# Optimization experiments

Measured on AMD Instinct MI355X. Metric: run time of the kernel, lower is better.

The kernel has to match this reference:

```python
import jax, jax.numpy as jnp
import numpy as np

B, T, C = 2, 2048, 1024
NH = 16
DFF = 4096
EPS = 1e-5


def setup_inputs() -> dict:
    key = jax.random.key(0)
    ks = jax.random.split(key, 12)
    s = 0.02
    return {
        "x": jax.random.normal(ks[0], (B, T, C), dtype=jnp.float32),
        "Wq": jax.random.normal(ks[1], (C, C), dtype=jnp.float32) * s,
        "bq": jax.random.normal(ks[2], (C,), dtype=jnp.float32) * s,
        "Wk": jax.random.normal(ks[3], (C, C), dtype=jnp.float32) * s,
        "bk": jax.random.normal(ks[4], (C,), dtype=jnp.float32) * s,
        "Wv": jax.random.normal(ks[5], (C, C), dtype=jnp.float32) * s,
        "bv": jax.random.normal(ks[6], (C,), dtype=jnp.float32) * s,
        "W1": jax.random.normal(ks[7], (C, DFF), dtype=jnp.float32) * s,
        "b1": jax.random.normal(ks[8], (DFF,), dtype=jnp.float32) * s,
        "W2": jax.random.normal(ks[9], (DFF, C), dtype=jnp.float32) * s,
        "b2": jax.random.normal(ks[10], (C,), dtype=jnp.float32) * s,
        "ln_w": jnp.ones((C,), dtype=jnp.float32),
    }


def _layernorm(x, w):
    # LayerNorm over last dim, weight only (bias=False), eps=1e-5
    mu = jnp.mean(x, axis=-1, keepdims=True)
    var = jnp.mean(jnp.square(x - mu), axis=-1, keepdims=True)
    return (x - mu) / jnp.sqrt(var + EPS) * w


def reference(x, Wq, bq, Wk, bk, Wv, bv, W1, b1, W2, b2, ln_w):
    Bx, Tx, Cx = x.shape
    hd = Cx // NH
    q = (x @ Wq + bq).reshape(Bx, Tx, NH, hd).transpose(0, 2, 1, 3)  # [B,H,T,hd]
    k = (x @ Wk + bk).reshape(Bx, Tx, NH, hd).transpose(0, 2, 1, 3)
    v = (x @ Wv + bv).reshape(Bx, Tx, NH, hd).transpose(0, 2, 1, 3)
    # NOTE: original scales by sqrt(d_k) = sqrt(FULL model dim C), not head dim
    scores = jnp.einsum("bhqd,bhkd->bhqk", q, k) / jnp.sqrt(jnp.float32(Cx))
    causal = jnp.tril(jnp.ones((Tx, Tx), dtype=bool))
    scores = jnp.where(causal[None, None, :, :], scores, -jnp.inf)
    attn = jax.nn.softmax(scores, axis=-1)
    head_out = jnp.einsum("bhqk,bhkd->bhqd", attn, v)
    a = head_out.transpose(0, 2, 1, 3).reshape(Bx, Tx, Cx)
    # residuals: out = x + ln(x) with SHARED ln weight
    h = a + _layernorm(a, ln_w)
    f = jax.nn.relu(h @ W1 + b1) @ W2 + b2
    out = f + _layernorm(f, ln_w)
    return out
```

## Files before the change

kernel.cpp:

```cpp
#include <hip/hip_runtime.h>
#include <math.h>


typedef __attribute__((ext_vector_type(8))) short short8;
typedef __attribute__((ext_vector_type(4))) float f32x4;

__device__ __forceinline__ unsigned short f2bf(float f) {
    unsigned u = __builtin_bit_cast(unsigned, f);
    unsigned r = u + 0x7fffu + ((u >> 16) & 1u);
    return (unsigned short)(r >> 16);
}

__global__ __launch_bounds__(256) void prep_kernel(
    const float* __restrict__ x,  const float* __restrict__ Wq,
    const float* __restrict__ Wk, const float* __restrict__ Wv,
    const float* __restrict__ W1, const float* __restrict__ W2,
    const float* __restrict__ bq, const float* __restrict__ bk,
    unsigned short* __restrict__ x_bf,  unsigned short* __restrict__ Wqk_t,
    unsigned short* __restrict__ Wvt,   unsigned short* __restrict__ W1t,
    unsigned short* __restrict__ W2t,   float* __restrict__ bqk)
{
    const int bid = blockIdx.x;
    const int tid = threadIdx.x;

    if (bid < 4096) {
        const int i = (bid * 256 + tid) * 4;
        float4 v = *(const float4*)(x + i);
        ushort4 o;
        o.x = f2bf(v.x); o.y = f2bf(v.y); o.z = f2bf(v.z); o.w = f2bf(v.w);
        *(ushort4*)(x_bf + i) = o;
        return;
    }
    if (bid >= 15360) {
        const int i = (bid - 15360) * 256 + tid;
        bqk[i] = i < 1024 ? bq[i] : bk[i - 1024];
        return;
    }

    __shared__ float tile[32][33];
    const float* src; unsigned short* dst; int K, N, t;
    if (bid < 5120)       { t = bid - 4096;  src = Wq; dst = Wqk_t;            K = 1024; N = 1024; }
    else if (bid < 6144)  { t = bid - 5120;  src = Wk; dst = Wqk_t + 1048576;  K = 1024; N = 1024; }
    else if (bid < 7168)  { t = bid - 6144;  src = Wv; dst = Wvt;              K = 1024; N = 1024; }
    else if (bid < 11264) { t = bid - 7168;  src = W1; dst = W1t;              K = 1024; N = 4096; }
    else                  { t = bid - 11264; src = W2; dst = W2t;              K = 4096; N = 1024; }

    const int ncols = N >> 5;
    const int n0 = (t % ncols) * 32;
    const int k0 = (t / ncols) * 32;
    const int tx = tid & 31;
    const int ty = tid >> 5;
#pragma unroll
    for (int i = 0; i < 4; ++i)
        tile[ty + i * 8][tx] = src[(size_t)(k0 + ty + i * 8) * N + n0 + tx];
    __syncthreads();
#pragma unroll
    for (int i = 0; i < 4; ++i)
        dst[(size_t)(n0 + ty + i * 8) * K + k0 + tx] = f2bf(tile[tx][ty + i * 8]);
}

template <int TM, int TN, int NP>
__device__ __forceinline__ void gemm_body(
    unsigned short* AsB, unsigned short* BsB,
    const unsigned short* __restrict__ A, const unsigned short* __restrict__ Bt,
    const float* __restrict__ bias, float* __restrict__ Cf,
    unsigned short* __restrict__ Cb, int M, int N, int K, int mode,
    int bx, int by)
{
    constexpr int NI   = TM / 32;
    constexpr int NJ   = TN / 32;
    constexpr int NCA  = TM / 16;
    constexpr int NCB  = TN / 16;
    constexpr int MAXA = (NCA + 3) / 4;
    constexpr int MAXB = (NCB + 3) / 4;

    const int tid  = threadIdx.x;
    const int lane = tid & 63;
    const int w    = tid >> 6;
    const int wm   = (w & 1) * (TM / 2);
    const int wn   = (w >> 1) * (TN / 2);
    const int fm   = lane & 15;
    const int quad = lane >> 4;

    const int row0 = by * TM;
    const int col0 = bx * TN;

    const int srow = lane >> 2;
    const int scol = (lane & 3) * 8;

    const unsigned short* aptr[MAXA];
    int aoff[MAXA];
#pragma unroll
    for (int i = 0; i < MAXA; ++i) {
        const int c = w + i * 4;
        if (c < NCA) {
            aptr[i] = A + (size_t)(row0 + c * 16 + srow) * K + scol;
            aoff[i] = c * 16 * 32;
        }
    }
    const unsigned short* bptr[MAXB];
    int boff[MAXB];
#pragma unroll
    for (int i = 0; i < MAXB; ++i) {
        const int c = w + i * 4;
        if (c < NCB) {
            bptr[i] = Bt + (size_t)(col0 + c * 16 + srow) * K + scol;
            boff[i] = c * 16 * 32;
        }
    }

    f32x4 acc[NI][NJ] = {};

    for (int k0 = 0; k0 < K; k0 += NP * 32) {
        __syncthreads();
#pragma unroll
        for (int p = 0; p < NP; ++p) {
#pragma unroll
            for (int i = 0; i < MAXA; ++i)
                if (w + i * 4 < NCA)
                    __builtin_amdgcn_global_load_lds(
                        (const __attribute__((address_space(1))) void*)(aptr[i] + k0 + p * 32),
                        (__attribute__((address_space(3))) void*)&AsB[p * TM * 32 + aoff[i]], 16, 0, 0);
#pragma unroll
            for (int i = 0; i < MAXB; ++i)
                if (w + i * 4 < NCB)
                    __builtin_amdgcn_global_load_lds(
                        (const __attribute__((address_space(1))) void*)(bptr[i] + k0 + p * 32),
                        (__attribute__((address_space(3))) void*)&BsB[p * TN * 32 + boff[i]], 16, 0, 0);
        }
        __syncthreads();

#pragma unroll
        for (int p = 0; p < NP; ++p) {
            short8 af[NI], bf[NJ];
#pragma unroll
            for (int i = 0; i < NI; ++i)
                af[i] = *(const short8*)&AsB[p * TM * 32 + (wm + i * 16 + fm) * 32 + quad * 8];
#pragma unroll
            for (int j = 0; j < NJ; ++j)
                bf[j] = *(const short8*)&BsB[p * TN * 32 + (wn + j * 16 + fm) * 32 + quad * 8];
#pragma unroll
            for (int i = 0; i < NI; ++i)
#pragma unroll
                for (int j = 0; j < NJ; ++j)
                    acc[i][j] = __builtin_amdgcn_mfma_f32_16x16x32_bf16(
                        af[i], bf[j], acc[i][j], 0, 0, 0);
        }
    }

#pragma unroll
    for (int j = 0; j < NJ; ++j) {
        const int col = col0 + wn + j * 16 + fm;
        const float bcol = (mode == 3) ? 0.f : bias[col];
#pragma unroll
        for (int i = 0; i < NI; ++i) {
            const int rbase = row0 + wm + i * 16 + quad * 4;
#pragma unroll
            for (int r = 0; r < 4; ++r) {
                const int row = rbase + r;
                float val = acc[i][j][r] + ((mode == 3) ? bias[row] : bcol);
                if (mode == 1) val = fmaxf(val, 0.f);
                if (mode == 0) Cf[(size_t)row * N + col] = val;
                else           Cb[(size_t)row * N + col] = f2bf(val);
            }
        }
    }
}

template <int TM, int TN, int NP>
__global__ __launch_bounds__(256) void gemm_bf16_mfma(
    const unsigned short* __restrict__ A, const unsigned short* __restrict__ Bt,
    const float* __restrict__ bias, float* __restrict__ Cf,
    unsigned short* __restrict__ Cb, int M, int N, int K, int mode)
{
    __shared__ unsigned short As[NP * TM * 32];
    __shared__ unsigned short Bs[NP * TN * 32];
    gemm_body<TM, TN, NP>(As, Bs, A, Bt, bias, Cf, Cb, M, N, K, mode,
                          blockIdx.x, blockIdx.y);
}

template <int TM, int TN, int NP>
__global__ __launch_bounds__(256) void gemm_xcd(
    const unsigned short* __restrict__ A, const unsigned short* __restrict__ Bt,
    const float* __restrict__ bias, float* __restrict__ Cf,
    unsigned short* __restrict__ Cb, int M, int N, int K, int mode,
    int nx, int rows_per_xcd)
{
    __shared__ unsigned short As[NP * TM * 32];
    __shared__ unsigned short Bs[NP * TN * 32];
    const int xcd = blockIdx.x & 7;
    const int idx = blockIdx.x >> 3;
    const int bx  = idx % nx;
    const int by  = xcd * rows_per_xcd + idx / nx;
    gemm_body<TM, TN, NP>(As, Bs, A, Bt, bias, Cf, Cb, M, N, K, mode, bx, by);
}

template <int TM, int TN, int NP>
__global__ __launch_bounds__(256) void gemm_dual(
    const unsigned short* __restrict__ A0, const unsigned short* __restrict__ B0,
    const float* __restrict__ bias0, unsigned short* __restrict__ C0,
    int M0, int N0, int K0, int mode0, int nb0, int nx0,
    const unsigned short* __restrict__ A1, const unsigned short* __restrict__ B1,
    const float* __restrict__ bias1, unsigned short* __restrict__ C1,
    int M1, int N1, int K1, int mode1, int nx1)
{
    __shared__ unsigned short As[NP * TM * 32];
    __shared__ unsigned short Bs[NP * TN * 32];
    const int bid = blockIdx.x;
    if (bid < nb0) {
        gemm_body<TM, TN, NP>(As, Bs, A0, B0, bias0, nullptr, C0,
                              M0, N0, K0, mode0, bid % nx0, bid / nx0);
    } else {
        const int t = bid - nb0;
        gemm_body<TM, TN, NP>(As, Bs, A1, B1, bias1, nullptr, C1,
                              M1, N1, K1, mode1, t % nx1, t / nx1);
    }
}

__global__ __launch_bounds__(256) void fattn_mfma(
    const unsigned short* __restrict__ qk,
    const unsigned short* __restrict__ vt,
    float* __restrict__ a)
{
    const int T = 2048, LDQK = 2048, LDVT = 4096, OUTC = 1024;
    const float cs = 0.04508422f;

    __shared__ unsigned short Qs[2][64][32];
    __shared__ unsigned short Ks[2][64][32];
    __shared__ unsigned short Vs[2][64][32];
    __shared__ unsigned short Ps[4][16][72];

    const int tid  = threadIdx.x;
    const int lane = tid & 63;
    const int w    = tid >> 6;
    const int fm   = lane & 15;
    const int quad = lane >> 4;
    const int srow = lane >> 2;
    const int scol = (lane & 3) * 8;

    const int n  = blockIdx.x;
    const int lo = n & 255, hi = n >> 8;
    const int h  = ((lo >> 5) & 7) | ((hi & 1) << 3);
    const int b  = hi >> 1;
    const int qv = lo & 31;
    const int u  = ((qv & 1) << 4) | ((qv & 2) << 2) | (qv & 4) |
                   ((qv & 8) >> 2) | ((qv & 16) >> 4);
    const int qb = (hi & 1) ? (31 - u) : u;
    const int q0 = qb * 64;

    const size_t rowbase = (size_t)b * T;

#pragma unroll
    for (int i = 0; i < 2; ++i) {
        const int c  = w * 2 + i;
        const int kh = c & 1, rg = c >> 1;
        const unsigned short* src = qk + (rowbase + q0 + rg * 16 + srow) * LDQK
                                       + h * 64 + kh * 32 + scol;
        __builtin_amdgcn_global_load_lds(
            (const __attribute__((address_space(1))) void*)src,
            (__attribute__((address_space(3))) void*)&Qs[kh][rg * 16][0], 16, 0, 0);
    }
    __syncthreads();
    short8 qf0 = *(const short8*)&Qs[0][w * 16 + fm][quad * 8];
    short8 qf1 = *(const short8*)&Qs[1][w * 16 + fm][quad * 8];

    short8 ones;
#pragma unroll
    for (int i = 0; i < 8; ++i) ones[i] = (short)0x3F80;

    f32x4 o[4] = {};
    f32x4 lacc = {};

    const int qglob = q0 + w * 16 + fm;

    for (int jt = 0; jt <= qb; ++jt) {
        const int j0 = jt * 64;
        __syncthreads();
#pragma unroll
        for (int i = 0; i < 2; ++i) {
            const int c  = w * 2 + i;
            const int kh = c & 1, rg = c >> 1;
            const unsigned short* ksrc = qk + (rowbase + j0 + rg * 16 + srow) * LDQK
                                            + 1024 + h * 64 + kh * 32 + scol;
            __builtin_amdgcn_global_load_lds(
                (const __attribute__((address_space(1))) void*)ksrc,
                (__attribute__((address_space(3))) void*)&Ks[kh][rg * 16][0], 16, 0, 0);
            const unsigned short* vsrc = vt + (size_t)(h * 64 + rg * 16 + srow) * LDVT
                                            + rowbase + j0 + kh * 32 + scol;
            __builtin_amdgcn_global_load_lds(
                (const __attribute__((address_space(1))) void*)vsrc,
                (__attribute__((address_space(3))) void*)&Vs[kh][rg * 16][0], 16, 0, 0);
        }
        __syncthreads();

        f32x4 s[4];
#pragma unroll
        for (int j = 0; j < 4; ++j) {
            short8 k0 = *(const short8*)&Ks[0][j * 16 + fm][quad * 8];
            short8 k1 = *(const short8*)&Ks[1][j * 16 + fm][quad * 8];
            f32x4 acc = {};
            acc = __builtin_amdgcn_mfma_f32_16x16x32_bf16(k0, qf0, acc, 0, 0, 0);
            acc = __builtin_amdgcn_mfma_f32_16x16x32_bf16(k1, qf1, acc, 0, 0, 0);
            s[j] = acc;
        }

        if (jt == qb) {
#pragma unroll
            for (int j = 0; j < 4; ++j) {
                const int kbase = j0 + j * 16 + quad * 4;
#pragma unroll
                for (int r = 0; r < 4; ++r) {
                    const float e = exp2f(s[j][r] * cs);
                    s[j][r] = (kbase + r > qglob) ? 0.f : e;
                }
            }
        } else {
#pragma unroll
            for (int j = 0; j < 4; ++j)
#pragma unroll
                for (int r = 0; r < 4; ++r)
                    s[j][r] = exp2f(s[j][r] * cs);
        }

#pragma unroll
        for (int j = 0; j < 4; ++j) {
            const unsigned d0 = (unsigned)f2bf(s[j][0]) | ((unsigned)f2bf(s[j][1]) << 16);
            const unsigned d1 = (unsigned)f2bf(s[j][2]) | ((unsigned)f2bf(s[j][3]) << 16);
            *(uint2*)&Ps[w][fm][j * 16 + quad * 4] = make_uint2(d0, d1);
        }
        short8 pf0 = *(const short8*)&Ps[w][fm][quad * 8];
        short8 pf1 = *(const short8*)&Ps[w][fm][32 + quad * 8];

#pragma unroll
        for (int jd = 0; jd < 4; ++jd) {
            short8 v0 = *(const short8*)&Vs[0][jd * 16 + fm][quad * 8];
            short8 v1 = *(const short8*)&Vs[1][jd * 16 + fm][quad * 8];
            o[jd] = __builtin_amdgcn_mfma_f32_16x16x32_bf16(pf0, v0, o[jd], 0, 0, 0);
            o[jd] = __builtin_amdgcn_mfma_f32_16x16x32_bf16(pf1, v1, o[jd], 0, 0, 0);
        }
        lacc = __builtin_amdgcn_mfma_f32_16x16x32_bf16(pf0, ones, lacc, 0, 0, 0);
        lacc = __builtin_amdgcn_mfma_f32_16x16x32_bf16(pf1, ones, lacc, 0, 0, 0);
    }

    const size_t orow = rowbase + q0 + w * 16 + quad * 4;
#pragma unroll
    for (int r = 0; r < 4; ++r) {
        const float inv = 1.0f / lacc[r];
#pragma unroll
        for (int jd = 0; jd < 4; ++jd)
            a[(orow + r) * OUTC + h * 64 + jd * 16 + fm] = o[jd][r] * inv;
    }
}

__global__ __launch_bounds__(256) void add_ln_kernel(
    const float* __restrict__ in, const float* __restrict__ w,
    float* __restrict__ outf, unsigned short* __restrict__ outb, int bf16_out)
{
    const int C = 1024;
    const int row = blockIdx.x;
    const int tid = threadIdx.x;

    __shared__ float red[256];

    const float* x = in + (size_t)row * C;
    float4 xv = *(const float4*)(x + tid * 4);

    red[tid] = xv.x + xv.y + xv.z + xv.w;
    __syncthreads();
    for (int off = 128; off > 0; off >>= 1) {
        if (tid < off) red[tid] += red[tid + off];
        __syncthreads();
    }
    const float mu = red[0] * (1.0f / 1024.0f);
    __syncthreads();

    float dx = xv.x - mu, dy = xv.y - mu, dz = xv.z - mu, dw = xv.w - mu;
    red[tid] = dx * dx + dy * dy + dz * dz + dw * dw;
    __syncthreads();
    for (int off = 128; off > 0; off >>= 1) {
        if (tid < off) red[tid] += red[tid + off];
        __syncthreads();
    }
    const float rstd = rsqrtf(red[0] * (1.0f / 1024.0f) + 1e-5f);

    float4 wv = *(const float4*)(w + tid * 4);
    float ox = xv.x + dx * rstd * wv.x;
    float oy = xv.y + dy * rstd * wv.y;
    float oz = xv.z + dz * rstd * wv.z;
    float ow = xv.w + dw * rstd * wv.w;
    if (bf16_out) {
        ushort4 o4;
        o4.x = f2bf(ox); o4.y = f2bf(oy); o4.z = f2bf(oz); o4.w = f2bf(ow);
        *(ushort4*)(outb + (size_t)row * C + tid * 4) = o4;
    } else {
        *(float4*)(outf + (size_t)row * C + tid * 4) = make_float4(ox, oy, oz, ow);
    }
}

extern "C" void kernel_launch(void* const* d_in, const int* in_sizes, int n_in,
                              void* d_out, int out_size, void* d_ws, size_t ws_size,
                              hipStream_t stream)
{
    const float* x    = (const float*)d_in[0];
    const float* Wq   = (const float*)d_in[1];
    const float* bq   = (const float*)d_in[2];
    const float* Wk   = (const float*)d_in[3];
    const float* bk   = (const float*)d_in[4];
    const float* Wv   = (const float*)d_in[5];
    const float* bv   = (const float*)d_in[6];
    const float* W1   = (const float*)d_in[7];
    const float* b1   = (const float*)d_in[8];
    const float* W2   = (const float*)d_in[9];
    const float* b2   = (const float*)d_in[10];
    const float* ln_w = (const float*)d_in[11];
    float* out = (float*)d_out;
    char* ws = (char*)d_ws;

    const int B = 2, T = 2048, C = 1024, DFF = 4096;
    const int M = B * T;
    const size_t MB = 1048576;

    unsigned short* qk_bf = (unsigned short*)(ws);
    unsigned short* vt_bf = (unsigned short*)(ws + 16 * MB);
    float*          a     = (float*)(ws + 24 * MB);
    unsigned short* x_bf  = (unsigned short*)(ws + 40 * MB);
    unsigned short* Wqk_t = (unsigned short*)(ws + 48 * MB);
    unsigned short* Wvt   = (unsigned short*)(ws + 52 * MB);
    unsigned short* W1t   = (unsigned short*)(ws + 54 * MB);
    unsigned short* W2t   = (unsigned short*)(ws + 62 * MB);
    float*          bqk   = (float*)(ws + 70 * MB);
    unsigned short* u_bf  = (unsigned short*)(ws + 71 * MB);
    unsigned short* h_bf  = x_bf;
    float*          f     = (float*)(ws);

    dim3 blk(256);

    prep_kernel<<<dim3(15368), blk, 0, stream>>>(
        x, Wq, Wk, Wv, W1, W2, bq, bk,
        x_bf, Wqk_t, Wvt, W1t, W2t, bqk);

    gemm_dual<64, 64, 2><<<dim3(3072), blk, 0, stream>>>(
        x_bf, Wqk_t, bqk, qk_bf, M, 2 * C, C, 2, 2048, 32,
        Wvt, x_bf, bv, vt_bf, C, M, C, 3, 64);

    fattn_mfma<<<dim3(1024), blk, 0, stream>>>(qk_bf, vt_bf, a);

    add_ln_kernel<<<dim3(M), blk, 0, stream>>>(a, ln_w, nullptr, h_bf, 1);

    gemm_bf16_mfma<64, 128, 2><<<dim3(DFF / 128, M / 64), blk, 0, stream>>>(
        h_bf, W1t, b1, nullptr, u_bf, M, DFF, C, 1);

    gemm_xcd<128, 64, 4><<<dim3(512), blk, 0, stream>>>(
        u_bf, W2t, b2, f, nullptr, M, C, DFF, 0, 16, 4);

    add_ln_kernel<<<dim3(M), blk, 0, stream>>>(f, ln_w, out, nullptr, 0);
}
```

Before: 332.4 us.

## Enlarge GEMM tiles, add XCD-aware 2D tiling and split-K for FFN down projection

All GEMMs move to 128x128 tiles. The up projection gets an XCD-aware rectangular block mapping so each chiplet reuses a compact region of A and B. The down projection is split into two K halves that write separate fp32 buffers, and the final LayerNorm sums those halves before normalizing. The goal is more MFMA work per LDS load and better L2 locality, at the cost of fewer blocks per GEMM and an extra fp32 partial buffer to read and write.

```diff
diff --git a/kernel.cpp b/kernel.cpp
--- a/kernel.cpp
+++ b/kernel.cpp
@@ -65,7 +65,7 @@
     const unsigned short* __restrict__ A, const unsigned short* __restrict__ Bt,
     const float* __restrict__ bias, float* __restrict__ Cf,
     unsigned short* __restrict__ Cb, int M, int N, int K, int mode,
-    int bx, int by)
+    int bx, int by, int kbeg, int kend)
 {
     constexpr int NI   = TM / 32;
     constexpr int NJ   = TN / 32;
@@ -111,7 +111,7 @@
 
     f32x4 acc[NI][NJ] = {};
 
-    for (int k0 = 0; k0 < K; k0 += NP * 32) {
+    for (int k0 = kbeg; k0 < kend; k0 += NP * 32) {
         __syncthreads();
 #pragma unroll
         for (int p = 0; p < NP; ++p) {
@@ -151,7 +151,7 @@
 #pragma unroll
     for (int j = 0; j < NJ; ++j) {
         const int col = col0 + wn + j * 16 + fm;
-        const float bcol = (mode == 3) ? 0.f : bias[col];
+        const float bcol = (mode == 3 || mode == 4) ? 0.f : bias[col];
 #pragma unroll
         for (int i = 0; i < NI; ++i) {
             const int rbase = row0 + wm + i * 16 + quad * 4;
@@ -160,39 +160,50 @@
                 const int row = rbase + r;
                 float val = acc[i][j][r] + ((mode == 3) ? bias[row] : bcol);
                 if (mode == 1) val = fmaxf(val, 0.f);
-                if (mode == 0) Cf[(size_t)row * N + col] = val;
-                else           Cb[(size_t)row * N + col] = f2bf(val);
+                if (mode == 0 || mode == 4) Cf[(size_t)row * N + col] = val;
+                else                        Cb[(size_t)row * N + col] = f2bf(val);
             }
         }
     }
 }
 
 template <int TM, int TN, int NP>
-__global__ __launch_bounds__(256) void gemm_bf16_mfma(
-    const unsigned short* __restrict__ A, const unsigned short* __restrict__ Bt,
-    const float* __restrict__ bias, float* __restrict__ Cf,
-    unsigned short* __restrict__ Cb, int M, int N, int K, int mode)
-{
-    __shared__ unsigned short As[NP * TM * 32];
-    __shared__ unsigned short Bs[NP * TN * 32];
-    gemm_body<TM, TN, NP>(As, Bs, A, Bt, bias, Cf, Cb, M, N, K, mode,
-                          blockIdx.x, blockIdx.y);
-}
-
-template <int TM, int TN, int NP>
-__global__ __launch_bounds__(256) void gemm_xcd(
+__global__ __launch_bounds__(256) void gemm_xcd2(
     const unsigned short* __restrict__ A, const unsigned short* __restrict__ Bt,
     const float* __restrict__ bias, float* __restrict__ Cf,
     unsigned short* __restrict__ Cb, int M, int N, int K, int mode,
-    int nx, int rows_per_xcd)
+    int rw, int rh, int nrx)
 {
     __shared__ unsigned short As[NP * TM * 32];
     __shared__ unsigned short Bs[NP * TN * 32];
     const int xcd = blockIdx.x & 7;
     const int idx = blockIdx.x >> 3;
-    const int bx  = idx % nx;
-    const int by  = xcd * rows_per_xcd + idx / nx;
-    gemm_body<TM, TN, NP>(As, Bs, A, Bt, bias, Cf, Cb, M, N, K, mode, bx, by);
+    const int rx  = xcd % nrx;
+    const int ry  = xcd / nrx;
+    const int bx  = rx * rw + idx % rw;
+    const int by  = ry * rh + idx / rw;
+    gemm_body<TM, TN, NP>(As, Bs, A, Bt, bias, Cf, Cb, M, N, K, mode,
+                          bx, by, 0, K);
+}
+
+template <int TM, int TN, int NP>
+__global__ __launch_bounds__(256) void gemm_splitk(
+    const unsigned short* __restrict__ A, const unsigned short* __restrict__ Bt,
+    const float* __restrict__ bias, float* __restrict__ C0,
+    float* __restrict__ C1, int M, int N, int K,
+    int nxh, int rows_per_xcd_h, int nbh)
+{
+    __shared__ unsigned short As[NP * TM * 32];
+    __shared__ unsigned short Bs[NP * TN * 32];
+    const int half = blockIdx.x >= nbh;
+    const int r    = blockIdx.x - (half ? nbh : 0);
+    const int xcd  = blockIdx.x & 7;
+    const int idx  = r >> 3;
+    const int bx   = idx % nxh;
+    const int by   = xcd * rows_per_xcd_h + idx / nxh;
+    const int kb   = half ? (K >> 1) : 0;
+    gemm_body<TM, TN, NP>(As, Bs, A, Bt, bias, half ? C1 : C0, nullptr,
+                          M, N, K, half ? 4 : 0, bx, by, kb, kb + (K >> 1));
 }
 
 template <int TM, int TN, int NP>
@@ -209,11 +220,11 @@
     const int bid = blockIdx.x;
     if (bid < nb0) {
         gemm_body<TM, TN, NP>(As, Bs, A0, B0, bias0, nullptr, C0,
-                              M0, N0, K0, mode0, bid % nx0, bid / nx0);
+                              M0, N0, K0, mode0, bid % nx0, bid / nx0, 0, K0);
     } else {
         const int t = bid - nb0;
         gemm_body<TM, TN, NP>(As, Bs, A1, B1, bias1, nullptr, C1,
-                              M1, N1, K1, mode1, t % nx1, t / nx1);
+                              M1, N1, K1, mode1, t % nx1, t / nx1, 0, K1);
     }
 }
 
@@ -353,7 +364,8 @@
 }
 
 __global__ __launch_bounds__(256) void add_ln_kernel(
-    const float* __restrict__ in, const float* __restrict__ w,
+    const float* __restrict__ in, const float* __restrict__ in2,
+    const float* __restrict__ w,
     float* __restrict__ outf, unsigned short* __restrict__ outb, int bf16_out)
 {
     const int C = 1024;
@@ -364,6 +376,10 @@
 
     const float* x = in + (size_t)row * C;
     float4 xv = *(const float4*)(x + tid * 4);
+    if (in2) {
+        float4 yv = *(const float4*)(in2 + (size_t)row * C + tid * 4);
+        xv.x += yv.x; xv.y += yv.y; xv.z += yv.z; xv.w += yv.w;
+    }
 
     red[tid] = xv.x + xv.y + xv.z + xv.w;
     __syncthreads();
@@ -432,6 +448,7 @@
     unsigned short* u_bf  = (unsigned short*)(ws + 71 * MB);
     unsigned short* h_bf  = x_bf;
     float*          f     = (float*)(ws);
+    float*          f2    = a;
 
     dim3 blk(256);
 
@@ -439,19 +456,19 @@
         x, Wq, Wk, Wv, W1, W2, bq, bk,
         x_bf, Wqk_t, Wvt, W1t, W2t, bqk);
 
-    gemm_dual<64, 64, 2><<<dim3(3072), blk, 0, stream>>>(
-        x_bf, Wqk_t, bqk, qk_bf, M, 2 * C, C, 2, 2048, 32,
-        Wvt, x_bf, bv, vt_bf, C, M, C, 3, 64);
+    gemm_dual<128, 128, 2><<<dim3(768), blk, 0, stream>>>(
+        x_bf, Wqk_t, bqk, qk_bf, M, 2 * C, C, 2, 512, 16,
+        Wvt, x_bf, bv, vt_bf, C, M, C, 3, 32);
 
     fattn_mfma<<<dim3(1024), blk, 0, stream>>>(qk_bf, vt_bf, a);
 
-    add_ln_kernel<<<dim3(M), blk, 0, stream>>>(a, ln_w, nullptr, h_bf, 1);
-
-    gemm_bf16_mfma<64, 128, 2><<<dim3(DFF / 128, M / 64), blk, 0, stream>>>(
-        h_bf, W1t, b1, nullptr, u_bf, M, DFF, C, 1);
-
-    gemm_xcd<128, 64, 4><<<dim3(512), blk, 0, stream>>>(
-        u_bf, W2t, b2, f, nullptr, M, C, DFF, 0, 16, 4);
-
-    add_ln_kernel<<<dim3(M), blk, 0, stream>>>(f, ln_w, out, nullptr, 0);
-}
+    add_ln_kernel<<<dim3(M), blk, 0, stream>>>(a, nullptr, ln_w, nullptr, h_bf, 1);
+
+    gemm_xcd2<128, 128, 2><<<dim3(1024), blk, 0, stream>>>(
+        h_bf, W1t, b1, nullptr, u_bf, M, DFF, C, 1, 16, 8, 2);
+
+    gemm_splitk<128, 128, 2><<<dim3(512), blk, 0, stream>>>(
+        u_bf, W2t, b2, f, f2, M, C, DFF, 8, 4, 256);
+
+    add_ln_kernel<<<dim3(M), blk, 0, stream>>>(f, f2, ln_w, out, nullptr, 0);
+}
```

New measurement: 336.8 us. Within noise of the previous version (+1.3%).

## Double-buffer GEMM LDS tiles to overlap global loads with MFMA

Applied to the files above, without the earlier changes.

Converts the shared GEMM body from a single LDS buffer with two barriers per K step to a ping-pong double buffer. The next K slice is issued via global_load_lds while MFMAs run on the current one, leaving one barrier per step. LDS per block doubles, and the W2 GEMM's NP drops from 4 to 2 so its footprint stays the same. The add_ln kernel gains an unused optional second input. The loads into the next buffer may not be explicitly waited on before the barrier, so correctness relies on how the compiler handles that wait.

```diff
diff --git a/kernel.cpp b/kernel.cpp
--- a/kernel.cpp
+++ b/kernel.cpp
@@ -61,7 +61,7 @@
 
 template <int TM, int TN, int NP>
 __device__ __forceinline__ void gemm_body(
-    unsigned short* AsB, unsigned short* BsB,
+    unsigned short* As, unsigned short* Bs,
     const unsigned short* __restrict__ A, const unsigned short* __restrict__ Bt,
     const float* __restrict__ bias, float* __restrict__ Cf,
     unsigned short* __restrict__ Cb, int M, int N, int K, int mode,
@@ -73,6 +73,9 @@
     constexpr int NCB  = TN / 16;
     constexpr int MAXA = (NCA + 3) / 4;
     constexpr int MAXB = (NCB + 3) / 4;
+    constexpr int ASZ  = NP * TM * 32;
+    constexpr int BSZ  = NP * TN * 32;
+    constexpr int STEP = NP * 32;
 
     const int tid  = threadIdx.x;
     const int lane = tid & 63;
@@ -109,10 +112,7 @@
         }
     }
 
-    f32x4 acc[NI][NJ] = {};
-
-    for (int k0 = 0; k0 < K; k0 += NP * 32) {
-        __syncthreads();
+    auto stage = [&](int k0, unsigned short* Ab, unsigned short* Bb) {
 #pragma unroll
         for (int p = 0; p < NP; ++p) {
 #pragma unroll
@@ -120,25 +120,37 @@
                 if (w + i * 4 < NCA)
                     __builtin_amdgcn_global_load_lds(
                         (const __attribute__((address_space(1))) void*)(aptr[i] + k0 + p * 32),
-                        (__attribute__((address_space(3))) void*)&AsB[p * TM * 32 + aoff[i]], 16, 0, 0);
+                        (__attribute__((address_space(3))) void*)&Ab[p * TM * 32 + aoff[i]], 16, 0, 0);
 #pragma unroll
             for (int i = 0; i < MAXB; ++i)
                 if (w + i * 4 < NCB)
                     __builtin_amdgcn_global_load_lds(
                         (const __attribute__((address_space(1))) void*)(bptr[i] + k0 + p * 32),
-                        (__attribute__((address_space(3))) void*)&BsB[p * TN * 32 + boff[i]], 16, 0, 0);
-        }
-        __syncthreads();
+                        (__attribute__((address_space(3))) void*)&Bb[p * TN * 32 + boff[i]], 16, 0, 0);
+        }
+    };
+
+    f32x4 acc[NI][NJ] = {};
+
+    unsigned short* Ac = As;        unsigned short* Bc = Bs;
+    unsigned short* An = As + ASZ;  unsigned short* Bn = Bs + BSZ;
+
+    stage(0, Ac, Bc);
+    __syncthreads();
+
+    for (int k0 = 0; k0 < K; k0 += STEP) {
+        const int kn = k0 + STEP;
+        if (kn < K) stage(kn, An, Bn);
 
 #pragma unroll
         for (int p = 0; p < NP; ++p) {
             short8 af[NI], bf[NJ];
 #pragma unroll
             for (int i = 0; i < NI; ++i)
-                af[i] = *(const short8*)&AsB[p * TM * 32 + (wm + i * 16 + fm) * 32 + quad * 8];
+                af[i] = *(const short8*)&Ac[p * TM * 32 + (wm + i * 16 + fm) * 32 + quad * 8];
 #pragma unroll
             for (int j = 0; j < NJ; ++j)
-                bf[j] = *(const short8*)&BsB[p * TN * 32 + (wn + j * 16 + fm) * 32 + quad * 8];
+                bf[j] = *(const short8*)&Bc[p * TN * 32 + (wn + j * 16 + fm) * 32 + quad * 8];
 #pragma unroll
             for (int i = 0; i < NI; ++i)
 #pragma unroll
@@ -146,6 +158,11 @@
                     acc[i][j] = __builtin_amdgcn_mfma_f32_16x16x32_bf16(
                         af[i], bf[j], acc[i][j], 0, 0, 0);
         }
+
+        __syncthreads();
+        unsigned short* t;
+        t = Ac; Ac = An; An = t;
+        t = Bc; Bc = Bn; Bn = t;
     }
 
 #pragma unroll
@@ -173,8 +190,8 @@
     const float* __restrict__ bias, float* __restrict__ Cf,
     unsigned short* __restrict__ Cb, int M, int N, int K, int mode)
 {
-    __shared__ unsigned short As[NP * TM * 32];
-    __shared__ unsigned short Bs[NP * TN * 32];
+    __shared__ unsigned short As[2 * NP * TM * 32];
+    __shared__ unsigned short Bs[2 * NP * TN * 32];
     gemm_body<TM, TN, NP>(As, Bs, A, Bt, bias, Cf, Cb, M, N, K, mode,
                           blockIdx.x, blockIdx.y);
 }
@@ -186,8 +203,8 @@
     unsigned short* __restrict__ Cb, int M, int N, int K, int mode,
     int nx, int rows_per_xcd)
 {
-    __shared__ unsigned short As[NP * TM * 32];
-    __shared__ unsigned short Bs[NP * TN * 32];
+    __shared__ unsigned short As[2 * NP * TM * 32];
+    __shared__ unsigned short Bs[2 * NP * TN * 32];
     const int xcd = blockIdx.x & 7;
     const int idx = blockIdx.x >> 3;
     const int bx  = idx % nx;
@@ -204,8 +221,8 @@
     const float* __restrict__ bias1, unsigned short* __restrict__ C1,
     int M1, int N1, int K1, int mode1, int nx1)
 {
-    __shared__ unsigned short As[NP * TM * 32];
-    __shared__ unsigned short Bs[NP * TN * 32];
+    __shared__ unsigned short As[2 * NP * TM * 32];
+    __shared__ unsigned short Bs[2 * NP * TN * 32];
     const int bid = blockIdx.x;
     if (bid < nb0) {
         gemm_body<TM, TN, NP>(As, Bs, A0, B0, bias0, nullptr, C0,
@@ -353,7 +370,8 @@
 }
 
 __global__ __launch_bounds__(256) void add_ln_kernel(
-    const float* __restrict__ in, const float* __restrict__ w,
+    const float* __restrict__ in, const float* __restrict__ in2,
+    const float* __restrict__ w,
     float* __restrict__ outf, unsigned short* __restrict__ outb, int bf16_out)
 {
     const int C = 1024;
@@ -364,6 +382,10 @@
 
     const float* x = in + (size_t)row * C;
     float4 xv = *(const float4*)(x + tid * 4);
+    if (in2) {
+        float4 yv = *(const float4*)(in2 + (size_t)row * C + tid * 4);
+        xv.x += yv.x; xv.y += yv.y; xv.z += yv.z; xv.w += yv.w;
+    }
 
     red[tid] = xv.x + xv.y + xv.z + xv.w;
     __syncthreads();
@@ -445,13 +467,13 @@
 
     fattn_mfma<<<dim3(1024), blk, 0, stream>>>(qk_bf, vt_bf, a);
 
-    add_ln_kernel<<<dim3(M), blk, 0, stream>>>(a, ln_w, nullptr, h_bf, 1);
+    add_ln_kernel<<<dim3(M), blk, 0, stream>>>(a, nullptr, ln_w, nullptr, h_bf, 1);
 
     gemm_bf16_mfma<64, 128, 2><<<dim3(DFF / 128, M / 64), blk, 0, stream>>>(
         h_bf, W1t, b1, nullptr, u_bf, M, DFF, C, 1);
 
-    gemm_xcd<128, 64, 4><<<dim3(512), blk, 0, stream>>>(
+    gemm_xcd<128, 64, 2><<<dim3(512), blk, 0, stream>>>(
         u_bf, W2t, b2, f, nullptr, M, C, DFF, 0, 16, 4);
 
-    add_ln_kernel<<<dim3(M), blk, 0, stream>>>(f, ln_w, out, nullptr, 0);
-}
+    add_ln_kernel<<<dim3(M), blk, 0, stream>>>(f, nullptr, ln_w, out, nullptr, 0);
+}
```

Result: no change. 334.3 us (+0.6%).

## Triple-buffer GEMM LDS tiles with async global-to-LDS prefetch pipeline

Applied to the files above, without the earlier changes.

Rewrites the shared GEMM main loop as a three-stage software pipeline. Two k-steps are prefetched into LDS with global_load_lds, and each iteration waits only on the oldest loads with a counted vmcnt plus a single barrier before computing on that buffer. This replaces the two barriers per step and the exposed load latency of the old single-buffer loop. LDS use triples, which may cut occupancy, so the W2 GEMM's NP drops from 4 to 2 to keep its footprint in check.

```diff
diff --git a/kernel.cpp b/kernel.cpp
--- a/kernel.cpp
+++ b/kernel.cpp
@@ -61,7 +61,7 @@
 
 template <int TM, int TN, int NP>
 __device__ __forceinline__ void gemm_body(
-    unsigned short* AsB, unsigned short* BsB,
+    unsigned short* As, unsigned short* Bs,
     const unsigned short* __restrict__ A, const unsigned short* __restrict__ Bt,
     const float* __restrict__ bias, float* __restrict__ Cf,
     unsigned short* __restrict__ Cb, int M, int N, int K, int mode,
@@ -73,6 +73,10 @@
     constexpr int NCB  = TN / 16;
     constexpr int MAXA = (NCA + 3) / 4;
     constexpr int MAXB = (NCB + 3) / 4;
+    constexpr int ASZ  = NP * TM * 32;
+    constexpr int BSZ  = NP * TN * 32;
+    constexpr int STEP = NP * 32;
+    constexpr int LPW  = NP * (NCA + NCB) / 4;
 
     const int tid  = threadIdx.x;
     const int lane = tid & 63;
@@ -109,10 +113,7 @@
         }
     }
 
-    f32x4 acc[NI][NJ] = {};
-
-    for (int k0 = 0; k0 < K; k0 += NP * 32) {
-        __syncthreads();
+    auto stage = [&](int k0, unsigned short* Ab, unsigned short* Bb) {
 #pragma unroll
         for (int p = 0; p < NP; ++p) {
 #pragma unroll
@@ -120,25 +121,28 @@
                 if (w + i * 4 < NCA)
                     __builtin_amdgcn_global_load_lds(
                         (const __attribute__((address_space(1))) void*)(aptr[i] + k0 + p * 32),
-                        (__attribute__((address_space(3))) void*)&AsB[p * TM * 32 + aoff[i]], 16, 0, 0);
+                        (__attribute__((address_space(3))) void*)&Ab[p * TM * 32 + aoff[i]], 16, 0, 0);
 #pragma unroll
             for (int i = 0; i < MAXB; ++i)
                 if (w + i * 4 < NCB)
                     __builtin_amdgcn_global_load_lds(
                         (const __attribute__((address_space(1))) void*)(bptr[i] + k0 + p * 32),
-                        (__attribute__((address_space(3))) void*)&BsB[p * TN * 32 + boff[i]], 16, 0, 0);
-        }
-        __syncthreads();
-
+                        (__attribute__((address_space(3))) void*)&Bb[p * TN * 32 + boff[i]], 16, 0, 0);
+        }
+    };
+
+    f32x4 acc[NI][NJ] = {};
+
+    auto compute = [&](unsigned short* Ac, unsigned short* Bc) {
 #pragma unroll
         for (int p = 0; p < NP; ++p) {
             short8 af[NI], bf[NJ];
 #pragma unroll
             for (int i = 0; i < NI; ++i)
-                af[i] = *(const short8*)&AsB[p * TM * 32 + (wm + i * 16 + fm) * 32 + quad * 8];
+                af[i] = *(const short8*)&Ac[p * TM * 32 + (wm + i * 16 + fm) * 32 + quad * 8];
 #pragma unroll
             for (int j = 0; j < NJ; ++j)
-                bf[j] = *(const short8*)&BsB[p * TN * 32 + (wn + j * 16 + fm) * 32 + quad * 8];
+                bf[j] = *(const short8*)&Bc[p * TN * 32 + (wn + j * 16 + fm) * 32 + quad * 8];
 #pragma unroll
             for (int i = 0; i < NI; ++i)
 #pragma unroll
@@ -146,7 +150,28 @@
                     acc[i][j] = __builtin_amdgcn_mfma_f32_16x16x32_bf16(
                         af[i], bf[j], acc[i][j], 0, 0, 0);
         }
-    }
+    };
+
+    unsigned short *A0 = As, *A1 = As + ASZ, *A2 = As + 2 * ASZ;
+    unsigned short *B0 = Bs, *B1 = Bs + BSZ, *B2 = Bs + 2 * BSZ;
+
+    stage(0, A0, B0);
+    stage(STEP, A1, B1);
+
+    const int TSTEPS = K / STEP;
+    for (int t = 0; t < TSTEPS - 1; ++t) {
+        asm volatile("s_waitcnt vmcnt(%0)" :: "n"(LPW) : "memory");
+        __builtin_amdgcn_s_barrier();
+        const int k2 = (t + 2) * STEP;
+        if (k2 < K) stage(k2, A2, B2);
+        compute(A0, B0);
+        unsigned short* r;
+        r = A0; A0 = A1; A1 = A2; A2 = r;
+        r = B0; B0 = B1; B1 = B2; B2 = r;
+    }
+    asm volatile("s_waitcnt vmcnt(0)" ::: "memory");
+    __builtin_amdgcn_s_barrier();
+    compute(A0, B0);
 
 #pragma unroll
     for (int j = 0; j < NJ; ++j) {
@@ -173,8 +198,8 @@
     const float* __restrict__ bias, float* __restrict__ Cf,
     unsigned short* __restrict__ Cb, int M, int N, int K, int mode)
 {
-    __shared__ unsigned short As[NP * TM * 32];
-    __shared__ unsigned short Bs[NP * TN * 32];
+    __shared__ unsigned short As[3 * NP * TM * 32];
+    __shared__ unsigned short Bs[3 * NP * TN * 32];
     gemm_body<TM, TN, NP>(As, Bs, A, Bt, bias, Cf, Cb, M, N, K, mode,
                           blockIdx.x, blockIdx.y);
 }
@@ -186,8 +211,8 @@
     unsigned short* __restrict__ Cb, int M, int N, int K, int mode,
     int nx, int rows_per_xcd)
 {
-    __shared__ unsigned short As[NP * TM * 32];
-    __shared__ unsigned short Bs[NP * TN * 32];
+    __shared__ unsigned short As[3 * NP * TM * 32];
+    __shared__ unsigned short Bs[3 * NP * TN * 32];
     const int xcd = blockIdx.x & 7;
     const int idx = blockIdx.x >> 3;
     const int bx  = idx % nx;
@@ -204,8 +229,8 @@
     const float* __restrict__ bias1, unsigned short* __restrict__ C1,
     int M1, int N1, int K1, int mode1, int nx1)
 {
-    __shared__ unsigned short As[NP * TM * 32];
-    __shared__ unsigned short Bs[NP * TN * 32];
+    __shared__ unsigned short As[3 * NP * TM * 32];
+    __shared__ unsigned short Bs[3 * NP * TN * 32];
     const int bid = blockIdx.x;
     if (bid < nb0) {
         gemm_body<TM, TN, NP>(As, Bs, A0, B0, bias0, nullptr, C0,
@@ -450,7 +475,7 @@
     gemm_bf16_mfma<64, 128, 2><<<dim3(DFF / 128, M / 64), blk, 0, stream>>>(
         h_bf, W1t, b1, nullptr, u_bf, M, DFF, C, 1);
 
-    gemm_xcd<128, 64, 4><<<dim3(512), blk, 0, stream>>>(
+    gemm_xcd<128, 64, 2><<<dim3(512), blk, 0, stream>>>(
         u_bf, W2t, b2, f, nullptr, M, C, DFF, 0, 16, 4);
 
     add_ln_kernel<<<dim3(M), blk, 0, stream>>>(f, ln_w, out, nullptr, 0);
```

Result: slower. 359.3 us (+8.1%).
